# Kernel optimization log

Hardware: AMD Instinct MI355X
Metric: run time of the kernel (lower is better)

## Reference

```python
import jax, jax.numpy as jnp
import numpy as np

GRID = (32, 32, 32)  # must match init grid_size


def setup_inputs() -> dict:
    key = jax.random.key(0)
    # Mimic the module's init: D = 0.01 everywhere + 0.1 on the 6x6 diagonal,
    # plus small uniform noise so the baseline exercises non-degenerate values.
    D = jax.random.uniform(key, (6, 6, *GRID), dtype=jnp.float32) * 0.02 + 0.01
    D = D.at[jnp.arange(6), jnp.arange(6)].add(0.1)
    return {"D": D, "sx": 1, "sy": 1, "sz": 1, "ex": 30, "ey": 30, "ez": 30,
            "max_iterations": 300}


def reference(D, sx, sy, sz, ex, ey, ez, max_iterations):
    """flash_wave (training path, inference=False): 300-step CA as one lax.scan.

    Returns the stacked history of phi (pre-update, as the torch loop appends
    phi at the top of each iteration): shape [max_iterations, 6, X, Y, Z].
    Early exit is emulated by freezing phi once the wave reaches (ex,ey,ez),
    so no per-step host sync is needed.
    """
    phi0 = jnp.zeros((6, *GRID), dtype=D.dtype).at[:, sx, sy, sz].set(1.0)
    active_D = D + 0.95  # inference=False branch

    def body(carry, _):
        phi, done = carry
        # 6x6 channel mixing per grid cell: 'oixyz,ixyz->oxyz'
        phi_out = jnp.einsum('oixyz,ixyz->oxyz', active_D, phi)
        pn = jnp.zeros_like(phi)
        pn = pn.at[0, 1:, :, :].set(phi_out[0, :-1, :, :])   # +x
        pn = pn.at[1, :-1, :, :].set(phi_out[1, 1:, :, :])   # -x
        pn = pn.at[2, :, 1:, :].set(phi_out[2, :, :-1, :])   # +y
        pn = pn.at[3, :, :-1, :].set(phi_out[3, :, 1:, :])   # -y
        pn = pn.at[4, :, :, 1:].set(phi_out[4, :, :, :-1])   # +z
        pn = pn.at[5, :, :, :-1].set(phi_out[5, :, :, 1:])   # -z
        nxt = jnp.clip(pn, 0.0, 1.0)
        nxt = jnp.where(done, phi, nxt)  # freeze after target reached
        reached = jnp.sum(nxt[:, ex, ey, ez]) > 0.01
        return (nxt, jnp.logical_or(done, reached)), phi

    (_, _), history = jax.lax.scan(body, (phi0, jnp.array(False)), None,
                                   length=int(max_iterations))
    return history
```

## Files before the change

### kernel.cpp

```cpp
#include <hip/hip_runtime.h>

#define NCH 6
#define NX 32
#define PLANE 1024
#define NCELL (NX * PLANE)
#define STEP_STRIDE (NCH * NCELL)
#define NTHREADS 256
#define NBLOCKS 128
#define RB 2

#define RING_WORDS ((size_t)RB * 3 * NCELL)
#define F_DONE 0

typedef unsigned long long u64;

__device__ __forceinline__ u64 ld64(const u64* p) {
    return __hip_atomic_load(p, __ATOMIC_RELAXED, __HIP_MEMORY_SCOPE_SYSTEM);
}
__device__ __forceinline__ void st64(u64* p, u64 v) {
    __hip_atomic_store(p, v, __ATOMIC_RELAXED, __HIP_MEMORY_SCOPE_SYSTEM);
}
__device__ __forceinline__ int ldi(const int* p) {
    return __hip_atomic_load(p, __ATOMIC_RELAXED, __HIP_MEMORY_SCOPE_SYSTEM);
}
__device__ __forceinline__ void sti(int* p, int v) {
    __hip_atomic_store(p, v, __ATOMIC_RELAXED, __HIP_MEMORY_SCOPE_SYSTEM);
}
__device__ __forceinline__ u64 pack2p(float a, float b, unsigned P) {
    const u64 w = ((u64)__float_as_uint(b) << 32) | __float_as_uint(a);
    return P ? (w | 0x8000000080000000ULL) : w;
}
__device__ __forceinline__ bool tagok(u64 w, unsigned P) {
    return (((unsigned)(w >> 63)) == P) & ((((unsigned)w) >> 31) == P);
}
__device__ __forceinline__ void unpack2(u64 w, float* d0, float* d1) {
    *d0 = __uint_as_float((unsigned)w & 0x7fffffffu);
    *d1 = __uint_as_float((unsigned)(w >> 32) & 0x7fffffffu);
}

__global__ void __launch_bounds__(NTHREADS)
BEMNA_V7_2_PhaseSpace_44117904064519_kernel(
    const float* __restrict__ D,
    const int* __restrict__ sx_p, const int* __restrict__ sy_p,
    const int* __restrict__ sz_p, const int* __restrict__ ex_p,
    const int* __restrict__ ey_p, const int* __restrict__ ez_p,
    const int* __restrict__ maxit_p,
    float* __restrict__ out,
    u64* __restrict__ ring,
    int* __restrict__ flags)
{
    __shared__ float tile[2][NCH][NTHREADS];
    __shared__ int lds_dn;
    volatile int* vdn = &lds_dn;

    const int tid = (int)threadIdx.x;
    const int bx  = (int)blockIdx.x;
    const int x   = bx >> 2;
    const int s   = bx & 3;
    const int yl  = tid >> 5;
    const int z   = tid & 31;
    const int y   = (s << 3) + yl;
    const int cell = (x << 10) + (y << 5) + z;

    const int sx = *sx_p, sy = *sy_p, sz = *sz_p;
    const int ex = *ex_p, ey = *ey_p, ez = *ez_p;
    const int maxit = *maxit_p;
    const bool is_seed   = (cell == ((sx << 10) | (sy << 5) | sz));
    const bool is_target = (cell == ((ex << 10) | (ey << 5) | ez));

    const int  nbg[NCH] = { cell - PLANE, cell + PLANE, cell - 32, cell + 32, cell - 1, cell + 1 };
    const bool ok[NCH]  = { x >= 1, x <= 30, y >= 1, y <= 30, z >= 1, z <= 30 };
    const int izm = (tid - 1) & (NTHREADS - 1), izp = (tid + 1) & (NTHREADS - 1);

    const bool has_xm = (x >= 1), has_xp = (x <= 30);
    const bool has_ym = (yl == 0) && (y >= 1);
    const bool has_yp = (yl == 7) && (y <= 30);

    float dreg[NCH][NCH];
#pragma unroll
    for (int o = 0; o < NCH; ++o)
#pragma unroll
        for (int i = 0; i < NCH; ++i)
            dreg[o][i] = ok[o] ? D[(size_t)(o * NCH + i) * NCELL + nbg[o]] + 0.95f : 0.0f;

    const float iv = is_seed ? 1.0f : 0.0f;
    {
        const u64 p = pack2p(iv, iv, 0);
        st64(&ring[0 * NCELL + cell], p);
        st64(&ring[1 * NCELL + cell], p);
        st64(&ring[2 * NCELL + cell], p);
        float* outp = out + cell;
#pragma unroll
        for (int o = 0; o < NCH; ++o) { outp[o * NCELL] = iv; tile[0][o][tid] = iv; }
    }
    if (tid == 0) lds_dn = -1;
    __syncthreads();

    int tripped = 0;
    for (int t = 0; t <= maxit - 2; ++t) {
        const u64* r0 = ring + (size_t)(t & 1) * 3 * NCELL;
        const u64* r1 = r0 + NCELL;
        const u64* r2 = r1 + NCELL;
        const unsigned P = (unsigned)((t >> 1) & 1);
        const int cm = cell - PLANE, cp = cell + PLANE;
        const int am = cell - 32,    ap = cell + 32;

        u64 wa0 = 0, wa1 = 0, wa2 = 0, wb0 = 0, wb1 = 0, wb2 = 0;
        u64 wc0 = 0, wc1 = 0, wc2 = 0, wd0 = 0, wd1 = 0, wd2 = 0;
        for (;;) {
            if (has_xm) { wa0 = ld64(r0 + cm); wa1 = ld64(r1 + cm); wa2 = ld64(r2 + cm); }
            if (has_xp) { wb0 = ld64(r0 + cp); wb1 = ld64(r1 + cp); wb2 = ld64(r2 + cp); }
            if (has_ym) { wc0 = ld64(r0 + am); wc1 = ld64(r1 + am); wc2 = ld64(r2 + am); }
            if (has_yp) { wd0 = ld64(r0 + ap); wd1 = ld64(r1 + ap); wd2 = ld64(r2 + ap); }
            if ((tid & 63) == 0) {
                const int dn = ldi(&flags[F_DONE]);
                if (dn >= 0) *vdn = dn;
            }
            bool okr = true;
            if (has_xm) okr = okr & tagok(wa0, P) & tagok(wa1, P) & tagok(wa2, P);
            if (has_xp) okr = okr & tagok(wb0, P) & tagok(wb1, P) & tagok(wb2, P);
            if (has_ym) okr = okr & tagok(wc0, P) & tagok(wc1, P) & tagok(wc2, P);
            if (has_yp) okr = okr & tagok(wd0, P) & tagok(wd1, P) & tagok(wd2, P);
            const int d = *vdn;
            if (d >= 0 && t + 1 > d) break;
            if (__ballot(okr) == ~0ull) break;
            __builtin_amdgcn_s_sleep(1);
        }
        __syncthreads();
        { const int d = *vdn; if (d >= 0 && t + 1 > d) break; }

        float xm[NCH], xp[NCH], ym[NCH], yp[NCH];
        unpack2(wa0, &xm[0], &xm[1]); unpack2(wa1, &xm[2], &xm[3]); unpack2(wa2, &xm[4], &xm[5]);
        unpack2(wb0, &xp[0], &xp[1]); unpack2(wb1, &xp[2], &xp[3]); unpack2(wb2, &xp[4], &xp[5]);
        unpack2(wc0, &ym[0], &ym[1]); unpack2(wc1, &ym[2], &ym[3]); unpack2(wc2, &ym[4], &ym[5]);
        unpack2(wd0, &yp[0], &yp[1]); unpack2(wd1, &yp[2], &yp[3]); unpack2(wd2, &yp[4], &yp[5]);

        const float (*L)[NTHREADS] = tile[t & 1];
        if (!has_ym) {
            const int n = (tid - 32) & (NTHREADS - 1);
#pragma unroll
            for (int i = 0; i < NCH; ++i) ym[i] = L[i][n];
        }
        if (!has_yp) {
            const int n = (tid + 32) & (NTHREADS - 1);
#pragma unroll
            for (int i = 0; i < NCH; ++i) yp[i] = L[i][n];
        }

        float v[NCH];
        {
            float a0 = 0.f, a1 = 0.f, a2 = 0.f, a3 = 0.f, a4 = 0.f, a5 = 0.f;
#pragma unroll
            for (int i = 0; i < NCH; ++i) {
                a0 = fmaf(dreg[0][i], xm[i], a0);
                a1 = fmaf(dreg[1][i], xp[i], a1);
                a2 = fmaf(dreg[2][i], ym[i], a2);
                a3 = fmaf(dreg[3][i], yp[i], a3);
                a4 = fmaf(dreg[4][i], L[i][izm], a4);
                a5 = fmaf(dreg[5][i], L[i][izp], a5);
            }
            v[0] = fminf(fmaxf(a0, 0.f), 1.f);
            v[1] = fminf(fmaxf(a1, 0.f), 1.f);
            v[2] = fminf(fmaxf(a2, 0.f), 1.f);
            v[3] = fminf(fmaxf(a3, 0.f), 1.f);
            v[4] = fminf(fmaxf(a4, 0.f), 1.f);
            v[5] = fminf(fmaxf(a5, 0.f), 1.f);
        }

        if (is_target && !tripped) {
            if (v[0] + v[1] + v[2] + v[3] + v[4] + v[5] > 0.01f) {
                sti(&flags[F_DONE], t + 1);
                tripped = 1;
            }
        }

        {
            const unsigned P1 = (unsigned)(((t + 1) >> 1) & 1);
            u64* w0 = ring + (size_t)((t + 1) & 1) * 3 * NCELL;
            st64(w0 + 0 * NCELL + cell, pack2p(v[0], v[1], P1));
            st64(w0 + 1 * NCELL + cell, pack2p(v[2], v[3], P1));
            st64(w0 + 2 * NCELL + cell, pack2p(v[4], v[5], P1));
#pragma unroll
            for (int o = 0; o < NCH; ++o) tile[(t + 1) & 1][o][tid] = v[o];
        }

        {
            float* outp = out + (size_t)(t + 1) * STEP_STRIDE + cell;
#pragma unroll
            for (int o = 0; o < NCH; ++o) outp[o * NCELL] = v[o];
        }
    }
}

__global__ void fill_kernel(const int* __restrict__ flags,
                            float4* __restrict__ out,
                            int total4)
{
    const int s4 = STEP_STRIDE / 4;
    const int maxit = total4 / s4;
    const int ds = flags[F_DONE];
    const int tf = (ds >= 1 && ds <= maxit - 1) ? ds : maxit - 1;
    const int idx = (int)blockIdx.x * (int)blockDim.x + (int)threadIdx.x;
    const float4 v = out[(size_t)tf * s4 + idx];
    for (int t = tf + 1; t < maxit; ++t)
        out[(size_t)t * s4 + idx] = v;
}

extern "C" void kernel_launch(void* const* d_in, const int* in_sizes, int n_in,
                              void* d_out, int out_size, void* d_ws, size_t ws_size,
                              hipStream_t stream)
{
    const float* D   = (const float*)d_in[0];
    const int* sx    = (const int*)d_in[1];
    const int* sy    = (const int*)d_in[2];
    const int* sz    = (const int*)d_in[3];
    const int* ex    = (const int*)d_in[4];
    const int* ey    = (const int*)d_in[5];
    const int* ez    = (const int*)d_in[6];
    const int* maxit = (const int*)d_in[7];
    float* out = (float*)d_out;

    u64* ring  = (u64*)d_ws;
    int* flags = (int*)(ring + RING_WORDS);

    BEMNA_V7_2_PhaseSpace_44117904064519_kernel<<<dim3(NBLOCKS), dim3(NTHREADS), 0, stream>>>(
        D, sx, sy, sz, ex, ey, ez, maxit, out, ring, flags);

    const int total4 = out_size / 4;
    fill_kernel<<<dim3((STEP_STRIDE / 4) / 256), dim3(256), 0, stream>>>(
        flags, (float4*)out, total4);
}
```

Before: 402.6 us.

## Make each wavefront self-synchronizing via global tags, dropping LDS tile and block barrier

```diff
diff --git a/kernel.cpp b/kernel.cpp
--- a/kernel.cpp
+++ b/kernel.cpp
@@ -49,18 +49,12 @@
     u64* __restrict__ ring,
     int* __restrict__ flags)
 {
-    __shared__ float tile[2][NCH][NTHREADS];
-    __shared__ int lds_dn;
-    volatile int* vdn = &lds_dn;
-
-    const int tid = (int)threadIdx.x;
-    const int bx  = (int)blockIdx.x;
-    const int x   = bx >> 2;
-    const int s   = bx & 3;
-    const int yl  = tid >> 5;
-    const int z   = tid & 31;
-    const int y   = (s << 3) + yl;
-    const int cell = (x << 10) + (y << 5) + z;
+    const int tid  = (int)threadIdx.x;
+    const int cell = (int)blockIdx.x * NTHREADS + tid;
+    const int lane = tid & 63;
+    const int x = cell >> 10;
+    const int y = (cell >> 5) & 31;
+    const int z = cell & 31;
 
     const int sx = *sx_p, sy = *sy_p, sz = *sz_p;
     const int ex = *ex_p, ey = *ey_p, ez = *ez_p;
@@ -70,11 +64,12 @@
 
     const int  nbg[NCH] = { cell - PLANE, cell + PLANE, cell - 32, cell + 32, cell - 1, cell + 1 };
     const bool ok[NCH]  = { x >= 1, x <= 30, y >= 1, y <= 30, z >= 1, z <= 30 };
-    const int izm = (tid - 1) & (NTHREADS - 1), izp = (tid + 1) & (NTHREADS - 1);
-
-    const bool has_xm = (x >= 1), has_xp = (x <= 30);
-    const bool has_ym = (yl == 0) && (y >= 1);
-    const bool has_yp = (yl == 7) && (y <= 30);
+
+    const int cxm = ok[0] ? cell - PLANE : cell;
+    const int cxp = ok[1] ? cell + PLANE : cell;
+    const bool hi = (lane >= 32);
+    const int cye = hi ? (ok[3] ? cell + 32 : cell)
+                       : (ok[2] ? cell - 32 : cell);
 
     float dreg[NCH][NCH];
 #pragma unroll
@@ -83,6 +78,7 @@
         for (int i = 0; i < NCH; ++i)
             dreg[o][i] = ok[o] ? D[(size_t)(o * NCH + i) * NCELL + nbg[o]] + 0.95f : 0.0f;
 
+    float myv[NCH];
     const float iv = is_seed ? 1.0f : 0.0f;
     {
         const u64 p = pack2p(iv, iv, 0);
@@ -91,10 +87,8 @@
         st64(&ring[2 * NCELL + cell], p);
         float* outp = out + cell;
 #pragma unroll
-        for (int o = 0; o < NCH; ++o) { outp[o * NCELL] = iv; tile[0][o][tid] = iv; }
+        for (int o = 0; o < NCH; ++o) { myv[o] = iv; outp[o * NCELL] = iv; }
     }
-    if (tid == 0) lds_dn = -1;
-    __syncthreads();
 
     int tripped = 0;
     for (int t = 0; t <= maxit - 2; ++t) {
@@ -102,69 +96,58 @@
         const u64* r1 = r0 + NCELL;
         const u64* r2 = r1 + NCELL;
         const unsigned P = (unsigned)((t >> 1) & 1);
-        const int cm = cell - PLANE, cp = cell + PLANE;
-        const int am = cell - 32,    ap = cell + 32;
-
-        u64 wa0 = 0, wa1 = 0, wa2 = 0, wb0 = 0, wb1 = 0, wb2 = 0;
-        u64 wc0 = 0, wc1 = 0, wc2 = 0, wd0 = 0, wd1 = 0, wd2 = 0;
+
+        u64 a0, a1, a2, b0, b1, b2, c0, c1, c2;
+        int ab = 0;
         for (;;) {
-            if (has_xm) { wa0 = ld64(r0 + cm); wa1 = ld64(r1 + cm); wa2 = ld64(r2 + cm); }
-            if (has_xp) { wb0 = ld64(r0 + cp); wb1 = ld64(r1 + cp); wb2 = ld64(r2 + cp); }
-            if (has_ym) { wc0 = ld64(r0 + am); wc1 = ld64(r1 + am); wc2 = ld64(r2 + am); }
-            if (has_yp) { wd0 = ld64(r0 + ap); wd1 = ld64(r1 + ap); wd2 = ld64(r2 + ap); }
-            if ((tid & 63) == 0) {
-                const int dn = ldi(&flags[F_DONE]);
-                if (dn >= 0) *vdn = dn;
-            }
-            bool okr = true;
-            if (has_xm) okr = okr & tagok(wa0, P) & tagok(wa1, P) & tagok(wa2, P);
-            if (has_xp) okr = okr & tagok(wb0, P) & tagok(wb1, P) & tagok(wb2, P);
-            if (has_ym) okr = okr & tagok(wc0, P) & tagok(wc1, P) & tagok(wc2, P);
-            if (has_yp) okr = okr & tagok(wd0, P) & tagok(wd1, P) & tagok(wd2, P);
-            const int d = *vdn;
-            if (d >= 0 && t + 1 > d) break;
+            a0 = ld64(r0 + cxm); a1 = ld64(r1 + cxm); a2 = ld64(r2 + cxm);
+            b0 = ld64(r0 + cxp); b1 = ld64(r1 + cxp); b2 = ld64(r2 + cxp);
+            c0 = ld64(r0 + cye); c1 = ld64(r1 + cye); c2 = ld64(r2 + cye);
+            int dn = -1;
+            if (lane == 0) dn = ldi(&flags[F_DONE]);
+            dn = __shfl(dn, 0);
+            const bool okr = tagok(a0, P) & tagok(a1, P) & tagok(a2, P)
+                           & tagok(b0, P) & tagok(b1, P) & tagok(b2, P)
+                           & tagok(c0, P) & tagok(c1, P) & tagok(c2, P);
+            if (dn >= 0 && t + 1 > dn) { ab = 1; break; }
             if (__ballot(okr) == ~0ull) break;
             __builtin_amdgcn_s_sleep(1);
         }
-        __syncthreads();
-        { const int d = *vdn; if (d >= 0 && t + 1 > d) break; }
-
-        float xm[NCH], xp[NCH], ym[NCH], yp[NCH];
-        unpack2(wa0, &xm[0], &xm[1]); unpack2(wa1, &xm[2], &xm[3]); unpack2(wa2, &xm[4], &xm[5]);
-        unpack2(wb0, &xp[0], &xp[1]); unpack2(wb1, &xp[2], &xp[3]); unpack2(wb2, &xp[4], &xp[5]);
-        unpack2(wc0, &ym[0], &ym[1]); unpack2(wc1, &ym[2], &ym[3]); unpack2(wc2, &ym[4], &ym[5]);
-        unpack2(wd0, &yp[0], &yp[1]); unpack2(wd1, &yp[2], &yp[3]); unpack2(wd2, &yp[4], &yp[5]);
-
-        const float (*L)[NTHREADS] = tile[t & 1];
-        if (!has_ym) {
-            const int n = (tid - 32) & (NTHREADS - 1);
-#pragma unroll
-            for (int i = 0; i < NCH; ++i) ym[i] = L[i][n];
-        }
-        if (!has_yp) {
-            const int n = (tid + 32) & (NTHREADS - 1);
-#pragma unroll
-            for (int i = 0; i < NCH; ++i) yp[i] = L[i][n];
+        if (ab) break;
+
+        float xm[NCH], xp[NCH], ye[NCH];
+        unpack2(a0, &xm[0], &xm[1]); unpack2(a1, &xm[2], &xm[3]); unpack2(a2, &xm[4], &xm[5]);
+        unpack2(b0, &xp[0], &xp[1]); unpack2(b1, &xp[2], &xp[3]); unpack2(b2, &xp[4], &xp[5]);
+        unpack2(c0, &ye[0], &ye[1]); unpack2(c1, &ye[2], &ye[3]); unpack2(c2, &ye[4], &ye[5]);
+
+        float ym[NCH], yp[NCH], zm[NCH], zp[NCH];
+#pragma unroll
+        for (int i = 0; i < NCH; ++i) {
+            const float yin = __shfl(myv[i], lane ^ 32);
+            zm[i] = __shfl(myv[i], (lane - 1) & 63);
+            zp[i] = __shfl(myv[i], (lane + 1) & 63);
+            ym[i] = hi ? yin : ye[i];
+            yp[i] = hi ? ye[i] : yin;
         }
 
         float v[NCH];
         {
-            float a0 = 0.f, a1 = 0.f, a2 = 0.f, a3 = 0.f, a4 = 0.f, a5 = 0.f;
+            float s0 = 0.f, s1 = 0.f, s2 = 0.f, s3 = 0.f, s4 = 0.f, s5 = 0.f;
 #pragma unroll
             for (int i = 0; i < NCH; ++i) {
-                a0 = fmaf(dreg[0][i], xm[i], a0);
-                a1 = fmaf(dreg[1][i], xp[i], a1);
-                a2 = fmaf(dreg[2][i], ym[i], a2);
-                a3 = fmaf(dreg[3][i], yp[i], a3);
-                a4 = fmaf(dreg[4][i], L[i][izm], a4);
-                a5 = fmaf(dreg[5][i], L[i][izp], a5);
+                s0 = fmaf(dreg[0][i], xm[i], s0);
+                s1 = fmaf(dreg[1][i], xp[i], s1);
+                s2 = fmaf(dreg[2][i], ym[i], s2);
+                s3 = fmaf(dreg[3][i], yp[i], s3);
+                s4 = fmaf(dreg[4][i], zm[i], s4);
+                s5 = fmaf(dreg[5][i], zp[i], s5);
             }
-            v[0] = fminf(fmaxf(a0, 0.f), 1.f);
-            v[1] = fminf(fmaxf(a1, 0.f), 1.f);
-            v[2] = fminf(fmaxf(a2, 0.f), 1.f);
-            v[3] = fminf(fmaxf(a3, 0.f), 1.f);
-            v[4] = fminf(fmaxf(a4, 0.f), 1.f);
-            v[5] = fminf(fmaxf(a5, 0.f), 1.f);
+            v[0] = fminf(fmaxf(s0, 0.f), 1.f);
+            v[1] = fminf(fmaxf(s1, 0.f), 1.f);
+            v[2] = fminf(fmaxf(s2, 0.f), 1.f);
+            v[3] = fminf(fmaxf(s3, 0.f), 1.f);
+            v[4] = fminf(fmaxf(s4, 0.f), 1.f);
+            v[5] = fminf(fmaxf(s5, 0.f), 1.f);
         }
 
         if (is_target && !tripped) {
@@ -180,8 +163,6 @@
             st64(w0 + 0 * NCELL + cell, pack2p(v[0], v[1], P1));
             st64(w0 + 1 * NCELL + cell, pack2p(v[2], v[3], P1));
             st64(w0 + 2 * NCELL + cell, pack2p(v[4], v[5], P1));
-#pragma unroll
-            for (int o = 0; o < NCH; ++o) tile[(t + 1) & 1][o][tid] = v[o];
         }
 
         {
@@ -189,6 +170,8 @@
 #pragma unroll
             for (int o = 0; o < NCH; ++o) outp[o * NCELL] = v[o];
         }
+#pragma unroll
+        for (int o = 0; o < NCH; ++o) myv[o] = v[o];
     }
 }
 
```

Measured after the change: 406.6 us. Within noise of the previous version (+1.0%).
